# Performance work log

Measured on AMD Instinct MI355X. Metric: run time of the kernel, lower is better.

The kernel has to match this reference:

```python
import jax, jax.numpy as jnp
import numpy as np

T, IN, H, OUT = 4096, 1024, 1024, 512


def setup_inputs() -> dict:
    key = jax.random.key(0)
    ks = jax.random.split(key, 7)
    s_g = 1.0 / np.sqrt(H + IN)  # xavier-ish scale for gate weights
    s_y = 1.0 / np.sqrt(H)
    return {
        "x": jax.random.normal(ks[0], (T, IN), jnp.float32),
        "wf": jax.random.normal(ks[1], (H, H + IN), jnp.float32) * s_g,
        "bf": jnp.zeros((H,), jnp.float32),
        "wi": jax.random.normal(ks[2], (H, H + IN), jnp.float32) * s_g,
        "bi": jnp.zeros((H,), jnp.float32),
        "wc": jax.random.normal(ks[3], (H, H + IN), jnp.float32) * s_g,
        "bc": jnp.zeros((H,), jnp.float32),
        "wo": jax.random.normal(ks[4], (H, H + IN), jnp.float32) * s_g,
        "bo": jnp.zeros((H,), jnp.float32),
        "why": jax.random.normal(ks[5], (OUT, H), jnp.float32) * s_y,
        "by": jnp.zeros((OUT,), jnp.float32),
    }


def reference(x, wf, bf, wi, bi, wc, bc, wo, bo, why, by):
    hid = wf.shape[0]

    def step(carry, x_t):
        h, c = carry
        concat = jnp.concatenate([h, x_t])  # (H+IN,)
        f = jax.nn.sigmoid(wf @ concat + bf)
        i = jax.nn.sigmoid(wi @ concat + bi)
        o = jax.nn.sigmoid(wo @ concat + bo)
        g = jnp.tanh(wc @ concat + bc)
        c_new = f * c + i * g
        h_new = o * jnp.tanh(c_new)
        y = why @ h_new + by  # (OUT,)
        return (h_new, c_new), y

    h0 = jnp.zeros((hid,), x.dtype)
    c0 = jnp.zeros((hid,), x.dtype)
    (h, c), ys = jax.lax.scan(step, (h0, c0), x)
    return ys, h, c
```

## Files before the change

### kernel.cpp

```cpp
#include <hip/hip_runtime.h>
#include <stdint.h>

#define TT 4096
#define INW 1024
#define HW 1024
#define OUTW 512
#define CH 2048


__device__ __forceinline__ uint64_t pack_pair(float v, uint32_t ep) {
    return ((uint64_t)ep << 32) | (uint64_t)__float_as_uint(v);
}
__device__ __forceinline__ float sigmoid_fast(float z) {
    return 1.0f / (1.0f + __expf(-z));
}
__device__ __forceinline__ float tanh_fast(float z) {
    return 1.0f - 2.0f / (1.0f + __expf(2.0f * z));
}

__global__ void lstm_init_kernel(uint64_t* __restrict__ hpair) {
    int j = blockIdx.x * blockDim.x + threadIdx.x;
    if (j < HW) {
        hpair[j]      = pack_pair(0.0f, 0u);
        hpair[HW + j] = pack_pair(0.0f, 0x80000000u);
    }
}

__global__ __launch_bounds__(256, 1) void lstm_seq_kernel(
    const float* __restrict__ x,
    const float* __restrict__ wf, const float* __restrict__ bf,
    const float* __restrict__ wi, const float* __restrict__ bi,
    const float* __restrict__ wc, const float* __restrict__ bc,
    const float* __restrict__ wo, const float* __restrict__ bo,
    uint64_t* __restrict__ hpair, float* __restrict__ h_all,
    float* __restrict__ out)
{
    __shared__ float hsh[2][HW];

    const int tid  = threadIdx.x;
    const int lane = tid & 63;
    const int w    = tid >> 6;
    const int b    = blockIdx.x;
    const int gu   = b * 4 + w;

    float wh[64], wx[64];
    {
        const float* wptr[4] = {wf, wi, wc, wo};
#pragma unroll
        for (int g = 0; g < 4; ++g) {
            const float* base = wptr[g] + (size_t)gu * CH + lane;
#pragma unroll
            for (int k = 0; k < 16; ++k) wh[g * 16 + k] = base[(size_t)k * 64];
#pragma unroll
            for (int k = 0; k < 16; ++k) wx[g * 16 + k] = base[1024 + (size_t)k * 64];
        }
    }
#pragma unroll
    for (int i = 0; i < 64; ++i) {
        asm volatile("" : "+v"(wh[i]));
        asm volatile("" : "+v"(wx[i]));
    }

    const float bias0 = bf[gu];
    const float bias1 = bi[gu];
    const float bias2 = bc[gu];
    const float bias3 = bo[gu];

    float xv[16];
    {
        const float* xp = x + lane;
#pragma unroll
        for (int k = 0; k < 16; ++k) xv[k] = xp[(size_t)k * 64];
    }

    float c = 0.0f, h_last = 0.0f;

    for (int t = 0; t < TT; ++t) {
        float acc0 = 0.f, acc1 = 0.f, acc2 = 0.f, acc3 = 0.f;

#pragma unroll
        for (int k = 0; k < 16; ++k) {
            float v = xv[k];
            acc0 = fmaf(wx[0 * 16 + k], v, acc0);
            acc1 = fmaf(wx[1 * 16 + k], v, acc1);
            acc2 = fmaf(wx[2 * 16 + k], v, acc2);
            acc3 = fmaf(wx[3 * 16 + k], v, acc3);
        }

        const uint64_t* hp = hpair + (size_t)(t & 1) * HW + 256 * w + lane;
        float hq[4];
        {
            bool ok;
            do {
                uint64_t pv[4];
#pragma unroll
                for (int k = 0; k < 4; ++k)
                    pv[k] = __hip_atomic_load(&hp[64 * k],
                                              __ATOMIC_RELAXED, __HIP_MEMORY_SCOPE_SYSTEM);
                ok = true;
#pragma unroll
                for (int k = 0; k < 4; ++k)
                    ok &= ((uint32_t)(pv[k] >> 32) == (uint32_t)t);
#pragma unroll
                for (int k = 0; k < 4; ++k)
                    hq[k] = __uint_as_float((uint32_t)pv[k]);
            } while (!__all(ok));
        }

        float xn[16];
        {
            const float* xp = x + (size_t)(t + 1 < TT ? t + 1 : t) * INW + lane;
#pragma unroll
            for (int k = 0; k < 16; ++k) xn[k] = xp[(size_t)k * 64];
        }

#pragma unroll
        for (int k = 0; k < 4; ++k)
            hsh[t & 1][256 * w + lane + 64 * k] = hq[k];
        __syncthreads();

        if (t >= 1 && b == (t & 255)) {
            float4 hv4 = *(const float4*)&hsh[t & 1][tid * 4];
            *(float4*)(h_all + (size_t)(t - 1) * HW + tid * 4) = hv4;
        }

#pragma unroll
        for (int k = 0; k < 16; ++k) {
            float v = hsh[t & 1][lane + 64 * k];
            acc0 = fmaf(wh[0 * 16 + k], v, acc0);
            acc1 = fmaf(wh[1 * 16 + k], v, acc1);
            acc2 = fmaf(wh[2 * 16 + k], v, acc2);
            acc3 = fmaf(wh[3 * 16 + k], v, acc3);
        }

#pragma unroll
        for (int s = 32; s > 0; s >>= 1) {
            acc0 += __shfl_xor(acc0, s, 64);
            acc1 += __shfl_xor(acc1, s, 64);
            acc2 += __shfl_xor(acc2, s, 64);
            acc3 += __shfl_xor(acc3, s, 64);
        }

        float f  = sigmoid_fast(acc0 + bias0);
        float ii = sigmoid_fast(acc1 + bias1);
        float g  = tanh_fast(acc2 + bias2);
        float o  = sigmoid_fast(acc3 + bias3);
        c = fmaf(f, c, ii * g);
        float hn = o * tanh_fast(c);
        h_last = hn;

        if (lane == 0) {
            __hip_atomic_store(&hpair[(size_t)((t + 1) & 1) * HW + gu],
                               pack_pair(hn, (uint32_t)(t + 1)),
                               __ATOMIC_RELAXED, __HIP_MEMORY_SCOPE_SYSTEM);
        }

#pragma unroll
        for (int k = 0; k < 16; ++k) xv[k] = xn[k];
    }

    if (lane == 0) {
        h_all[(size_t)(TT - 1) * HW + gu] = h_last;
        out[(size_t)TT * OUTW + gu]      = h_last;
        out[(size_t)TT * OUTW + HW + gu] = c;
    }
}

__global__ __launch_bounds__(256) void lstm_ygemm_kernel(
    const float* __restrict__ hall, const float* __restrict__ why,
    const float* __restrict__ by, float* __restrict__ ys)
{
    __shared__ float hs[64][17];
    __shared__ float wsm[64][17];
    const int t0 = blockIdx.x * 64, o0 = blockIdx.y * 64;
    const int tid = threadIdx.x;
    const int tx = tid & 15, ty = tid >> 4;

    float acc[4][4] = {};
    const int r = tid >> 2;
    const int cc = (tid & 3) * 4;

    for (int kk = 0; kk < HW; kk += 16) {
        float4 hv = *(const float4*)(hall + (size_t)(t0 + r) * HW + kk + cc);
        hs[r][cc + 0] = hv.x; hs[r][cc + 1] = hv.y;
        hs[r][cc + 2] = hv.z; hs[r][cc + 3] = hv.w;
        float4 wv = *(const float4*)(why + (size_t)(o0 + r) * HW + kk + cc);
        wsm[r][cc + 0] = wv.x; wsm[r][cc + 1] = wv.y;
        wsm[r][cc + 2] = wv.z; wsm[r][cc + 3] = wv.w;
        __syncthreads();
#pragma unroll
        for (int k = 0; k < 16; ++k) {
            float ha[4], wa[4];
#pragma unroll
            for (int i = 0; i < 4; ++i) ha[i] = hs[ty * 4 + i][k];
#pragma unroll
            for (int j = 0; j < 4; ++j) wa[j] = wsm[tx * 4 + j][k];
#pragma unroll
            for (int i = 0; i < 4; ++i)
#pragma unroll
                for (int j = 0; j < 4; ++j)
                    acc[i][j] = fmaf(ha[i], wa[j], acc[i][j]);
        }
        __syncthreads();
    }
#pragma unroll
    for (int i = 0; i < 4; ++i) {
#pragma unroll
        for (int j = 0; j < 4; ++j) {
            int oo = o0 + tx * 4 + j;
            ys[(size_t)(t0 + ty * 4 + i) * OUTW + oo] = acc[i][j] + by[oo];
        }
    }
}

extern "C" void kernel_launch(void* const* d_in, const int* in_sizes, int n_in,
                              void* d_out, int out_size, void* d_ws, size_t ws_size,
                              hipStream_t stream) {
    const float* x   = (const float*)d_in[0];
    const float* wf  = (const float*)d_in[1];
    const float* bf  = (const float*)d_in[2];
    const float* wi  = (const float*)d_in[3];
    const float* bi  = (const float*)d_in[4];
    const float* wc  = (const float*)d_in[5];
    const float* bc  = (const float*)d_in[6];
    const float* wo  = (const float*)d_in[7];
    const float* bo  = (const float*)d_in[8];
    const float* why = (const float*)d_in[9];
    const float* by  = (const float*)d_in[10];
    float* out = (float*)d_out;

    uint64_t* hpair = (uint64_t*)d_ws;
    float* h_all = (float*)((char*)d_ws + (size_t)2 * HW * sizeof(uint64_t));

    lstm_init_kernel<<<dim3(4), dim3(256), 0, stream>>>(hpair);
    lstm_seq_kernel<<<dim3(256), dim3(256), 0, stream>>>(
        x, wf, bf, wi, bi, wc, bc, wo, bo, hpair, h_all, out);
    lstm_ygemm_kernel<<<dim3(64, 8), dim3(256), 0, stream>>>(h_all, why, by, out);
}
```

Measured before the change: 7.829 ms.

## Move next-step input projection off critical path and use DPP wave reduction

The x·W_x projection for step t+1 is now computed after the h-publish store, so it overlaps the wait for other blocks' hidden state instead of sitting between the wait and the recurrent matmul. The butterfly shuffle reduction is replaced with a DPP row/broadcast reduction that leaves the sum only in lane 63, and the gate math and store move to that lane. A sched_barrier keeps the compiler from hoisting the x work ahead of the store. This targets per-step latency in the serial recurrence loop, at the cost of slightly more register pressure and reliance on DPP control codes.

```diff
diff --git a/kernel.cpp b/kernel.cpp
--- a/kernel.cpp
+++ b/kernel.cpp
@@ -16,6 +16,21 @@
 }
 __device__ __forceinline__ float tanh_fast(float z) {
     return 1.0f - 2.0f / (1.0f + __expf(2.0f * z));
+}
+
+template <int CTRL>
+__device__ __forceinline__ float dpp_add(float v) {
+    int s = __builtin_amdgcn_update_dpp(0, __float_as_int(v), CTRL, 0xF, 0xF, true);
+    return v + __int_as_float(s);
+}
+__device__ __forceinline__ float wave_sum_to_lane63(float v) {
+    v = dpp_add<0x111>(v);
+    v = dpp_add<0x112>(v);
+    v = dpp_add<0x114>(v);
+    v = dpp_add<0x118>(v);
+    v = dpp_add<0x142>(v);
+    v = dpp_add<0x143>(v);
+    return v;
 }
 
 __global__ void lstm_init_kernel(uint64_t* __restrict__ hpair) {
@@ -66,28 +81,27 @@
     const float bias2 = bc[gu];
     const float bias3 = bo[gu];
 
-    float xv[16];
+    float xacc0 = 0.f, xacc1 = 0.f, xacc2 = 0.f, xacc3 = 0.f;
     {
         const float* xp = x + lane;
+        float xv[16];
 #pragma unroll
         for (int k = 0; k < 16; ++k) xv[k] = xp[(size_t)k * 64];
+#pragma unroll
+        for (int k = 0; k < 16; ++k) {
+            xacc0 = fmaf(wx[0 * 16 + k], xv[k], xacc0);
+            xacc1 = fmaf(wx[1 * 16 + k], xv[k], xacc1);
+            xacc2 = fmaf(wx[2 * 16 + k], xv[k], xacc2);
+            xacc3 = fmaf(wx[3 * 16 + k], xv[k], xacc3);
+        }
     }
 
     float c = 0.0f, h_last = 0.0f;
 
     for (int t = 0; t < TT; ++t) {
-        float acc0 = 0.f, acc1 = 0.f, acc2 = 0.f, acc3 = 0.f;
-
-#pragma unroll
-        for (int k = 0; k < 16; ++k) {
-            float v = xv[k];
-            acc0 = fmaf(wx[0 * 16 + k], v, acc0);
-            acc1 = fmaf(wx[1 * 16 + k], v, acc1);
-            acc2 = fmaf(wx[2 * 16 + k], v, acc2);
-            acc3 = fmaf(wx[3 * 16 + k], v, acc3);
-        }
-
-        const uint64_t* hp = hpair + (size_t)(t & 1) * HW + 256 * w + lane;
+        const int p = t & 1;
+
+        const uint64_t* hp = hpair + (size_t)p * HW + 256 * w + lane;
         float hq[4];
         {
             bool ok;
@@ -107,59 +121,65 @@
             } while (!__all(ok));
         }
 
+#pragma unroll
+        for (int k = 0; k < 4; ++k)
+            hsh[p][256 * w + lane + 64 * k] = hq[k];
+        __syncthreads();
+
         float xn[16];
         {
-            const float* xp = x + (size_t)(t + 1 < TT ? t + 1 : t) * INW + lane;
+            const int tn = (t + 1 < TT) ? t + 1 : t;
+            const float* xp = x + (size_t)tn * INW + lane;
 #pragma unroll
             for (int k = 0; k < 16; ++k) xn[k] = xp[(size_t)k * 64];
         }
 
-#pragma unroll
-        for (int k = 0; k < 4; ++k)
-            hsh[t & 1][256 * w + lane + 64 * k] = hq[k];
-        __syncthreads();
-
         if (t >= 1 && b == (t & 255)) {
-            float4 hv4 = *(const float4*)&hsh[t & 1][tid * 4];
+            float4 hv4 = *(const float4*)&hsh[p][tid * 4];
             *(float4*)(h_all + (size_t)(t - 1) * HW + tid * 4) = hv4;
         }
 
-#pragma unroll
-        for (int k = 0; k < 16; ++k) {
-            float v = hsh[t & 1][lane + 64 * k];
+        float acc0 = xacc0, acc1 = xacc1, acc2 = xacc2, acc3 = xacc3;
+#pragma unroll
+        for (int k = 0; k < 16; ++k) {
+            float v = hsh[p][lane + 64 * k];
             acc0 = fmaf(wh[0 * 16 + k], v, acc0);
             acc1 = fmaf(wh[1 * 16 + k], v, acc1);
             acc2 = fmaf(wh[2 * 16 + k], v, acc2);
             acc3 = fmaf(wh[3 * 16 + k], v, acc3);
         }
 
-#pragma unroll
-        for (int s = 32; s > 0; s >>= 1) {
-            acc0 += __shfl_xor(acc0, s, 64);
-            acc1 += __shfl_xor(acc1, s, 64);
-            acc2 += __shfl_xor(acc2, s, 64);
-            acc3 += __shfl_xor(acc3, s, 64);
-        }
-
-        float f  = sigmoid_fast(acc0 + bias0);
-        float ii = sigmoid_fast(acc1 + bias1);
-        float g  = tanh_fast(acc2 + bias2);
-        float o  = sigmoid_fast(acc3 + bias3);
-        c = fmaf(f, c, ii * g);
-        float hn = o * tanh_fast(c);
-        h_last = hn;
-
-        if (lane == 0) {
+        acc0 = wave_sum_to_lane63(acc0);
+        acc1 = wave_sum_to_lane63(acc1);
+        acc2 = wave_sum_to_lane63(acc2);
+        acc3 = wave_sum_to_lane63(acc3);
+
+        if (lane == 63) {
+            float f  = sigmoid_fast(acc0 + bias0);
+            float ii = sigmoid_fast(acc1 + bias1);
+            float g  = tanh_fast(acc2 + bias2);
+            float o  = sigmoid_fast(acc3 + bias3);
+            c = fmaf(f, c, ii * g);
+            float hn = o * tanh_fast(c);
+            h_last = hn;
             __hip_atomic_store(&hpair[(size_t)((t + 1) & 1) * HW + gu],
                                pack_pair(hn, (uint32_t)(t + 1)),
                                __ATOMIC_RELAXED, __HIP_MEMORY_SCOPE_SYSTEM);
         }
-
-#pragma unroll
-        for (int k = 0; k < 16; ++k) xv[k] = xn[k];
-    }
-
-    if (lane == 0) {
+        __builtin_amdgcn_sched_barrier(0);
+
+        float nx0 = 0.f, nx1 = 0.f, nx2 = 0.f, nx3 = 0.f;
+#pragma unroll
+        for (int k = 0; k < 16; ++k) {
+            nx0 = fmaf(wx[0 * 16 + k], xn[k], nx0);
+            nx1 = fmaf(wx[1 * 16 + k], xn[k], nx1);
+            nx2 = fmaf(wx[2 * 16 + k], xn[k], nx2);
+            nx3 = fmaf(wx[3 * 16 + k], xn[k], nx3);
+        }
+        xacc0 = nx0; xacc1 = nx1; xacc2 = nx2; xacc3 = nx3;
+    }
+
+    if (lane == 63) {
         h_all[(size_t)(TT - 1) * HW + gu] = h_last;
         out[(size_t)TT * OUTW + gu]      = h_last;
         out[(size_t)TT * OUTW + HW + gu] = c;
```

Result: faster. 6.757 ms (-13.7%).
